# Optimization experiments

Hardware: AMD Instinct MI355X
Metric: run time of the kernel (lower is better)

Reference implementation:

```python
import jax, jax.numpy as jnp
import numpy as np

MAX_PER_CLASS = 100   # max_num_boxes_per_class
MAX_TOTAL = 300       # max_num_boxes (pad_per_class=False -> output size is MAX_TOTAL)
IOU_THR = 0.5
SCORE_THR = 0.001
NEG = jnp.float32(-1e30)
EPS = 1e-12


def _canon(b):
    # boxes given as any diagonal pair (y1,x1,y2,x2); canonicalize like TF NMS
    ymin = jnp.minimum(b[..., 0], b[..., 2])
    ymax = jnp.maximum(b[..., 0], b[..., 2])
    xmin = jnp.minimum(b[..., 1], b[..., 3])
    xmax = jnp.maximum(b[..., 1], b[..., 3])
    return ymin, xmin, ymax, xmax


def _iou_one_vs_all(box, boxes):
    # box [4], boxes [N,4] -> iou [N]
    y1a, x1a, y2a, x2a = _canon(box)
    y1b, x1b, y2b, x2b = _canon(boxes)
    ih = jnp.maximum(jnp.minimum(y2a, y2b) - jnp.maximum(y1a, y1b), 0.0)
    iw = jnp.maximum(jnp.minimum(x2a, x2b) - jnp.maximum(x1a, x1b), 0.0)
    inter = ih * iw
    area_a = (y2a - y1a) * (x2a - x1a)
    area_b = (y2b - y1b) * (x2b - x1b)
    union = jnp.maximum(area_a + area_b - inter, EPS)
    return inter / union


def _nms_single_class(boxes_c, scores_c):
    # boxes_c [N,4], scores_c [N] -> (scores [K], boxes [K,4], valid [K]) with K=MAX_PER_CLASS
    N = scores_c.shape[0]
    valid = scores_c > SCORE_THR
    s = jnp.where(valid, scores_c, NEG)
    order = jnp.argsort(-s)
    b_sorted = boxes_c[order]          # [N,4]
    s_sorted = s[order]                # [N]
    v_sorted = valid[order]            # [N]

    def step(keep, xs):
        i, box_i, valid_i = xs
        iou_row = _iou_one_vs_all(box_i, b_sorted)          # [N]
        suppressed = jnp.any(keep & (iou_row > IOU_THR))    # vs previously kept only
        keep = keep.at[i].set(valid_i & jnp.logical_not(suppressed))
        return keep, None

    keep0 = jnp.zeros((N,), dtype=bool)
    keep, _ = jax.lax.scan(step, keep0, (jnp.arange(N), b_sorted, v_sorted))

    # cap number of kept boxes at MAX_PER_CLASS (in descending score order)
    rank = jnp.cumsum(keep.astype(jnp.int32)) - 1
    keep = keep & (rank < MAX_PER_CLASS)

    key = jnp.where(keep, s_sorted, NEG)
    top_s, top_i = jax.lax.top_k(key, MAX_PER_CLASS)
    top_boxes = b_sorted[top_i]
    top_valid = top_s > (NEG / 2)
    return top_s, top_boxes, top_valid


def _combined_nms(scores, boxes):
    # scores [B,N,C], boxes [B,N,q,4] with q==1 (boxes shared across classes)
    B, N, C = scores.shape
    q = boxes.shape[2]

    def per_image(scores_i, boxes_i):
        # scores_i [N,C], boxes_i [N,q,4]
        if q == 1:
            cls_boxes = jnp.broadcast_to(boxes_i, (N, C, 4))
        else:
            cls_boxes = boxes_i
        # per-class NMS, vmapped over the class axis
        sc, bx, vd = jax.vmap(_nms_single_class, in_axes=(1, 1))(cls_boxes, scores_i)
        # sc [C,K], bx [C,K,4], vd [C,K]
        cls_ids = jnp.broadcast_to(
            jnp.arange(C, dtype=scores.dtype)[:, None], vd.shape)

        flat_s = jnp.where(vd, sc, NEG).reshape(-1)   # [C*K]
        flat_b = bx.reshape(-1, 4)
        flat_c = cls_ids.reshape(-1)
        flat_v = vd.reshape(-1)

        top_s, idx = jax.lax.top_k(flat_s, MAX_TOTAL)
        out_v = flat_v[idx]
        out_s = jnp.where(out_v, top_s, 0.0)
        out_b = jnp.where(out_v[:, None], flat_b[idx], 0.0)
        out_b = jnp.clip(out_b, 0.0, 1.0)             # clip_boxes=True
        out_c = jnp.where(out_v, flat_c[idx], 0.0)
        count = jnp.sum(out_v.astype(jnp.int32))
        return out_s, out_b, out_c, count

    return jax.vmap(per_image)(scores, boxes)


def setup_inputs() -> dict:
    key = jax.random.key(0)
    k1, k2 = jax.random.split(key)
    B, N, C, Q = 4, 1024, 80, 1
    scores = jax.random.uniform(k1, (B, N, C), dtype=jnp.float32)
    boxes = jax.random.uniform(k2, (B, N, Q, 4), dtype=jnp.float32)
    return {"scores": scores, "boxes": boxes}


def reference(scores, boxes):
    # returns (output_scores, output_boxes, output_classes, valid_counts)
    return _combined_nms(scores, boxes)
```

## Files before the change

### kernel.cpp

```cpp
#include <hip/hip_runtime.h>
#include <stdint.h>

#define N_BOX 1024
#define C_CLS 80
#define B_IMG 4
#define K_PER 100
#define K_TOT 300
#define NEGF  (-1e30f)
#define NCAND (C_CLS * K_PER)
#define M_SEL 8192
#define KPAD  1088

#define OFF_WSCORE  1835008
#define OFF_WSIDX   1963008

typedef unsigned long long u64;
typedef unsigned int u32;

__device__ __forceinline__ int swz(int i) { return i + (i >> 4); }

__device__ __forceinline__ u32 ford(float f) {
    u32 u = __float_as_uint(f);
    return (u & 0x80000000u) ? ~u : (u | 0x80000000u);
}
__device__ __forceinline__ float funord(u32 o) {
    u32 u = (o & 0x80000000u) ? (o ^ 0x80000000u) : ~o;
    return __uint_as_float(u);
}

__device__ __forceinline__ bool iou_gt(float4 a, float aa, float4 b, float ab) {
#pragma clang fp contract(off)
    float ih = fminf(a.z, b.z) - fmaxf(a.x, b.x); ih = fmaxf(ih, 0.0f);
    float iw = fminf(a.w, b.w) - fmaxf(a.y, b.y); iw = fmaxf(iw, 0.0f);
    float inter = ih * iw;
    float uni = fmaxf(aa + ab - inter, 1e-12f);
    return (inter / uni) > 0.5f;
}

__global__ __launch_bounds__(256, 2) void nms_classes(
        const float* __restrict__ scores,
        const float* __restrict__ boxes,
        float* __restrict__ ws_score,
        int*   __restrict__ ws_idx)
{
    __shared__ u64    key[KPAD];
    __shared__ float4 bx[N_BOX];
    __shared__ float  ar[N_BOX];
    __shared__ float4 kb[K_PER];
    __shared__ float  ka[K_PER];
    __shared__ int    kept_t[K_PER];
    __shared__ u32    colk32[64][2];
    __shared__ u32    suppw[2];
    __shared__ int    sh_nvalid, sh_kept;

    const int tid  = threadIdx.x;
    const int lane = tid & 63;
    const int b  = blockIdx.x / C_CLS;
    const int c  = blockIdx.x % C_CLS;

    if (tid == 0) { sh_nvalid = 0; sh_kept = 0; }

    for (int n = tid; n < N_BOX; n += 256) {
        float4 v = ((const float4*)boxes)[b * N_BOX + n];
        {
#pragma clang fp contract(off)
            float y1 = fminf(v.x, v.z), y2 = fmaxf(v.x, v.z);
            float x1 = fminf(v.y, v.w), x2 = fmaxf(v.y, v.w);
            bx[n] = make_float4(y1, x1, y2, x2);
            ar[n] = (y2 - y1) * (x2 - x1);
        }
    }
    __syncthreads();

    u64 r[4];
    {
        const float* sc = scores + (size_t)(b * N_BOX) * C_CLS + c;
        int lv = 0;
        #pragma unroll
        for (int q = 0; q < 4; ++q) {
            int v = tid * 4 + q;
            float s0 = sc[(size_t)v * C_CLS];
            bool valid = s0 > 0.001f;
            float s = valid ? s0 : NEGF;
            r[q] = ((u64)ford(s) << 32) | (u32)(N_BOX - 1 - v);
            lv += valid ? 1 : 0;
        }
        if (lv) atomicAdd(&sh_nvalid, lv);
    }

    #define CE(a, b, d) { u64 _mx = (a) > (b) ? (a) : (b); \
                          u64 _mn = (a) > (b) ? (b) : (a); \
                          (a) = (d) ? _mx : _mn; (b) = (d) ? _mn : _mx; }
    CE(r[0], r[1], true); CE(r[2], r[3], false);

    for (int k = 4; k <= N_BOX; k <<= 1) {
        const bool d = ((tid & (k >> 2)) == 0);
        for (int j = k >> 1; j > 0; j >>= 1) {
            if (j >= 256) {
                __syncthreads();
                #pragma unroll
                for (int q = 0; q < 4; ++q) key[swz(tid * 4 + q)] = r[q];
                __syncthreads();
                const bool upper = ((tid * 4) & j) != 0;
                #pragma unroll
                for (int q = 0; q < 4; ++q) {
                    u64 pv = key[swz((tid * 4 + q) ^ j)];
                    u64 mx = r[q] > pv ? r[q] : pv;
                    u64 mn = r[q] > pv ? pv : r[q];
                    r[q] = (d != upper) ? mx : mn;
                }
            } else if (j >= 4) {
                const int dl = j >> 2;
                const bool upper = (lane & dl) != 0;
                #pragma unroll
                for (int q = 0; q < 4; ++q) {
                    u64 pv = __shfl_xor(r[q], dl);
                    u64 mx = r[q] > pv ? r[q] : pv;
                    u64 mn = r[q] > pv ? pv : r[q];
                    r[q] = (d != upper) ? mx : mn;
                }
            } else if (j == 2) {
                CE(r[0], r[2], d); CE(r[1], r[3], d);
            } else {
                CE(r[0], r[1], d); CE(r[2], r[3], d);
            }
        }
    }
    #undef CE

    __syncthreads();
    #pragma unroll
    for (int q = 0; q < 4; ++q) key[swz(tid * 4 + q)] = r[q];
    __syncthreads();

    const int nvalid = sh_nvalid;
    const int nwin = (nvalid + 63) >> 6;
    const int me  = tid & 63;
    const int grp = tid >> 6;

    for (int w = 0; w < nwin; ++w) {
        __syncthreads();
        if (sh_kept >= K_PER) break;
        const int kept0 = sh_kept;
        const int bt = w * 64;

        u64 kvm = key[swz((bt + me) & (N_BOX - 1))];
        int idxm = (N_BOX - 1) - (int)(u32)(kvm & 0xFFFFFFFFu);
        const float4 qm = bx[idxm];
        const float  am = ar[idxm];

        if (grp == 0) { colk32[me][0] = 0; colk32[me][1] = 0; }
        if (tid < 2) suppw[tid] = 0;
        __syncthreads();

        bool supme = false;
        for (int k = grp; k < kept0; k += 4)
            if (iou_gt(kb[k], ka[k], qm, am)) supme = true;
        if (supme) atomicOr(&suppw[me >> 5], 1u << (me & 31));

        u32 bits = 0;
        #pragma unroll
        for (int rq = 0; rq < 16; ++rq) {
            int rr = grp * 16 + rq;
            u64 kvr = key[swz((bt + rr) & (N_BOX - 1))];
            int idxr = (N_BOX - 1) - (int)(u32)(kvr & 0xFFFFFFFFu);
            bool kill = (rr != me) && iou_gt(bx[idxr], ar[idxr], qm, am);
            bits |= ((u32)kill) << rq;
        }
        atomicOr(&colk32[me][grp >> 1], bits << ((grp & 1) * 16));
        __syncthreads();

        if (grp == 0) {
            const u64 colkill = ((u64)colk32[lane][1] << 32) | colk32[lane][0];
            const u64 supp    = ((u64)suppw[1] << 32) | suppw[0];
            bool in = ((bt + lane) < nvalid) && !((supp >> lane) & 1ull);
            u64 pending = __ballot(in);
            int kept = kept0;
            while (pending && kept < K_PER) {
                int t0 = __ffsll((long long)pending) - 1;
                if (lane == 0) kept_t[kept] = bt + t0;
                if (lane == t0) { kb[kept] = qm; ka[kept] = am; }
                kept++;
                bool kill = (colkill >> t0) & 1ull;
                pending &= ~(1ull << t0);
                pending &= ~__ballot(kill);
            }
            if (lane == 0) sh_kept = kept;
        }
    }
    __syncthreads();

    const int kept = sh_kept;
    if (tid < K_PER) {
        int ob = (b * C_CLS + c) * K_PER + tid;
        if (tid < kept) {
            u64 k = key[swz(kept_t[tid])];
            ws_score[ob] = funord((u32)(k >> 32));
            ws_idx[ob]   = (N_BOX - 1) - (int)(u32)(k & 0xFFFFFFFFu);
        } else {
            ws_score[ob] = NEGF;
            ws_idx[ob]   = 0;
        }
    }
}

__global__ __launch_bounds__(1024) void final_topk(
        const float* __restrict__ ws_score,
        const int*   __restrict__ ws_idx,
        const float* __restrict__ boxes,
        float* __restrict__ out)
{
    __shared__ u32 skey[NCAND];
    __shared__ u32 hist4[256 * 4];
    __shared__ u64 list[512];
    __shared__ int sh_sel;
    __shared__ u32 sh_need;
    __shared__ int sh_cnt, sh_valid;

    const int tid = threadIdx.x;
    const int b = blockIdx.x;
    const int base = b * NCAND;

    if (tid == 0) { sh_cnt = 0; sh_valid = 0; }
    for (int i = tid; i < NCAND; i += 1024)
        skey[i] = ford(ws_score[base + i]);
    if (tid < 512) list[tid] = 0;
    hist4[tid] = 0;
    __syncthreads();

    u64 prefix = 0;
    u32 need = K_TOT;
    const int rounds[6] = {7, 6, 5, 4, 1, 0};
    const int slot = tid & 3;

    for (int rd = 0; rd < 6; ++rd) {
        const int d = rounds[rd];
        for (int i = tid; i < NCAND; i += 1024) {
            u64 k = ((u64)skey[i] << 32) | (u32)(M_SEL - 1 - i);
            bool match = (d == 7) || (((k ^ prefix) >> (8 * (d + 1))) == 0);
            if (match)
                atomicAdd(&hist4[(((u32)(k >> (8 * d)) & 0xFFu) << 2) | slot], 1u);
        }
        __syncthreads();
        if (tid < 64) {
            const int l = tid;
            u32 h[4];
            #pragma unroll
            for (int q = 0; q < 4; ++q) {
                int bin = 4 * l + q;
                h[q] = hist4[bin * 4 + 0] + hist4[bin * 4 + 1]
                     + hist4[bin * 4 + 2] + hist4[bin * 4 + 3];
                hist4[bin * 4 + 0] = 0; hist4[bin * 4 + 1] = 0;
                hist4[bin * 4 + 2] = 0; hist4[bin * 4 + 3] = 0;
            }
            u32 s3 = h[3], s2 = h[2] + s3, s1 = h[1] + s2, s0 = h[0] + s1;
            u32 tot = s0, S = tot;
            #pragma unroll
            for (int off = 1; off < 64; off <<= 1) {
                u32 t = __shfl(S, (l + off) & 63);
                if (l + off < 64) S += t;
            }
            u32 T = S - tot;
            u32 sv0 = s0 + T, sv1 = s1 + T, sv2 = s2 + T, sv3 = s3 + T;
            if (sv0 >= need && sv1 < need) { sh_sel = 4*l;     sh_need = need - sv1; }
            if (sv1 >= need && sv2 < need) { sh_sel = 4*l + 1; sh_need = need - sv2; }
            if (sv2 >= need && sv3 < need) { sh_sel = 4*l + 2; sh_need = need - sv3; }
            if (sv3 >= need && T   < need) { sh_sel = 4*l + 3; sh_need = need - T;   }
        }
        __syncthreads();
        prefix |= ((u64)(u32)sh_sel) << (8 * d);
        need = sh_need;
        __syncthreads();
    }

    for (int i = tid; i < NCAND; i += 1024) {
        u64 k = ((u64)skey[i] << 32) | (u32)(M_SEL - 1 - i);
        if (k >= prefix) {
            int p = atomicAdd(&sh_cnt, 1);
            if (p < 512) list[p] = k;
        }
    }
    __syncthreads();

    if (tid < 64) {
        const int l = tid;
        u64 e[8];
        #pragma unroll
        for (int q = 0; q < 8; ++q) e[q] = list[l * 8 + q];
        #define CE2(a, b, dd) { u64 _mx = (a) > (b) ? (a) : (b); \
                                u64 _mn = (a) > (b) ? (b) : (a); \
                                (a) = (dd) ? _mx : _mn; (b) = (dd) ? _mn : _mx; }
        CE2(e[0], e[1], true);  CE2(e[2], e[3], false);
        CE2(e[4], e[5], true);  CE2(e[6], e[7], false);
        CE2(e[0], e[2], true);  CE2(e[1], e[3], true);
        CE2(e[4], e[6], false); CE2(e[5], e[7], false);
        CE2(e[0], e[1], true);  CE2(e[2], e[3], true);
        CE2(e[4], e[5], false); CE2(e[6], e[7], false);
        for (int k = 8; k <= 512; k <<= 1) {
            const bool d = ((l & (k >> 3)) == 0);
            for (int j = k >> 1; j >= 8; j >>= 1) {
                const int dl = j >> 3;
                const bool upper = (l & dl) != 0;
                #pragma unroll
                for (int q = 0; q < 8; ++q) {
                    u64 pv = __shfl_xor(e[q], dl);
                    u64 mx = e[q] > pv ? e[q] : pv;
                    u64 mn = e[q] > pv ? pv : e[q];
                    e[q] = (d != upper) ? mx : mn;
                }
            }
            CE2(e[0], e[4], d); CE2(e[1], e[5], d);
            CE2(e[2], e[6], d); CE2(e[3], e[7], d);
            CE2(e[0], e[2], d); CE2(e[1], e[3], d);
            CE2(e[4], e[6], d); CE2(e[5], e[7], d);
            CE2(e[0], e[1], d); CE2(e[2], e[3], d);
            CE2(e[4], e[5], d); CE2(e[6], e[7], d);
        }
        #undef CE2
        #pragma unroll
        for (int q = 0; q < 8; ++q) list[l * 8 + q] = e[q];
    }
    __syncthreads();

    float* out_s = out;
    float* out_b = out + B_IMG * K_TOT;
    float* out_c = out + B_IMG * K_TOT * 5;
    float* out_n = out + B_IMG * K_TOT * 6;

    for (int i = tid; i < K_TOT; i += 1024) {
        u64 k = list[i];
        float s = funord((u32)(k >> 32));
        int flat = (M_SEL - 1) - (int)(u32)(k & 0xFFFFFFFFu);
        bool valid = s > (-5e29f);
        float os = 0.0f, oc = 0.0f;
        float4 ob = make_float4(0.0f, 0.0f, 0.0f, 0.0f);
        if (valid && flat < NCAND) {
            int cc = flat / K_PER;
            int n  = ws_idx[base + flat];
            float4 bb = ((const float4*)boxes)[b * N_BOX + n];
            os = s;
            oc = (float)cc;
            ob.x = fminf(fmaxf(bb.x, 0.0f), 1.0f);
            ob.y = fminf(fmaxf(bb.y, 0.0f), 1.0f);
            ob.z = fminf(fmaxf(bb.z, 0.0f), 1.0f);
            ob.w = fminf(fmaxf(bb.w, 0.0f), 1.0f);
            atomicAdd(&sh_valid, 1);
        }
        out_s[b * K_TOT + i] = os;
        ((float4*)out_b)[b * K_TOT + i] = ob;
        out_c[b * K_TOT + i] = oc;
    }
    __syncthreads();
    if (tid == 0) out_n[b] = (float)sh_valid;
}

extern "C" void kernel_launch(void* const* d_in, const int* in_sizes, int n_in,
                              void* d_out, int out_size, void* d_ws, size_t ws_size,
                              hipStream_t stream) {
    const float* scores = (const float*)d_in[0];
    const float* boxes  = (const float*)d_in[1];

    char* ws = (char*)d_ws;
    float* ws_score = (float*)(ws + OFF_WSCORE);
    int*   ws_idx   = (int*)  (ws + OFF_WSIDX);

    nms_classes<<<dim3(B_IMG * C_CLS), dim3(256), 0, stream>>>(
        scores, boxes, ws_score, ws_idx);
    final_topk<<<dim3(B_IMG), dim3(1024), 0, stream>>>(
        ws_score, ws_idx, boxes, (float*)d_out);
}
```

Baseline: 121.0 us.

## Double-buffer window boxes and replace shared atomics with ballots

Gathers the next window's sorted boxes into a double-buffered shared array while the current window runs, so the indirect key-to-box lookups leave the critical loop. Shared-memory atomics and the zeroing pass for the kill and suppress masks are replaced by per-wave plain stores and wave ballots, which removes one barrier per window. The suppression check against kept boxes is batched into groups of eight loads. The goal is fewer barriers and less LDS latency per window, in exchange for more shared memory and more register pressure.

```diff
diff --git a/kernel.cpp b/kernel.cpp
--- a/kernel.cpp
+++ b/kernel.cpp
@@ -46,11 +46,13 @@
     __shared__ u64    key[KPAD];
     __shared__ float4 bx[N_BOX];
     __shared__ float  ar[N_BOX];
-    __shared__ float4 kb[K_PER];
-    __shared__ float  ka[K_PER];
+    __shared__ float4 wb[2][64];
+    __shared__ float  wa[2][64];
+    __shared__ float4 kb[128];
+    __shared__ float  ka[128];
     __shared__ int    kept_t[K_PER];
-    __shared__ u32    colk32[64][2];
-    __shared__ u32    suppw[2];
+    __shared__ u32    colk16[4][64];
+    __shared__ u64    sup64[4];
     __shared__ int    sh_nvalid, sh_kept;
 
     const int tid  = threadIdx.x;
@@ -133,46 +135,78 @@
     for (int q = 0; q < 4; ++q) key[swz(tid * 4 + q)] = r[q];
     __syncthreads();
 
+    if (tid < 64) {
+        u64 kv = key[swz(tid)];
+        int idx = (N_BOX - 1) - (int)(u32)(kv & 0xFFFFFFFFu);
+        wb[0][tid] = bx[idx];
+        wa[0][tid] = ar[idx];
+    }
+
     const int nvalid = sh_nvalid;
     const int nwin = (nvalid + 63) >> 6;
     const int me  = tid & 63;
     const int grp = tid >> 6;
 
     for (int w = 0; w < nwin; ++w) {
+        const int cur = w & 1;
         __syncthreads();
         if (sh_kept >= K_PER) break;
         const int kept0 = sh_kept;
         const int bt = w * 64;
 
-        u64 kvm = key[swz((bt + me) & (N_BOX - 1))];
-        int idxm = (N_BOX - 1) - (int)(u32)(kvm & 0xFFFFFFFFu);
-        const float4 qm = bx[idxm];
-        const float  am = ar[idxm];
-
-        if (grp == 0) { colk32[me][0] = 0; colk32[me][1] = 0; }
-        if (tid < 2) suppw[tid] = 0;
+        if (grp == 1 && (w + 1) < nwin) {
+            u64 kv = key[swz((bt + 64 + me) & (N_BOX - 1))];
+            int idx = (N_BOX - 1) - (int)(u32)(kv & 0xFFFFFFFFu);
+            wb[cur ^ 1][me] = bx[idx];
+            wa[cur ^ 1][me] = ar[idx];
+        }
+
+        const float4 qm = wb[cur][me];
+        const float  am = wa[cur][me];
+
+        {
+            float4 wrow[16]; float warow[16];
+            #pragma unroll
+            for (int rq = 0; rq < 16; ++rq) {
+                wrow[rq]  = wb[cur][grp * 16 + rq];
+                warow[rq] = wa[cur][grp * 16 + rq];
+            }
+            u32 bits = 0;
+            #pragma unroll
+            for (int rq = 0; rq < 16; ++rq) {
+                int rr = grp * 16 + rq;
+                bool kill = (rr != me) && iou_gt(wrow[rq], warow[rq], qm, am);
+                bits |= ((u32)kill) << rq;
+            }
+            colk16[grp][me] = bits;
+        }
+
+        {
+            bool supme = false;
+            for (int t0 = 0; grp + 4 * t0 < kept0; t0 += 8) {
+                float4 kbl[8]; float kal[8];
+                #pragma unroll
+                for (int i = 0; i < 8; ++i) {
+                    int k = grp + 4 * (t0 + i);
+                    kbl[i] = kb[k]; kal[i] = ka[k];
+                }
+                #pragma unroll
+                for (int i = 0; i < 8; ++i) {
+                    int k = grp + 4 * (t0 + i);
+                    if (k < kept0 && iou_gt(kbl[i], kal[i], qm, am)) supme = true;
+                }
+            }
+            u64 bal = __ballot(supme);
+            if (lane == 0) sup64[grp] = bal;
+        }
         __syncthreads();
 
-        bool supme = false;
-        for (int k = grp; k < kept0; k += 4)
-            if (iou_gt(kb[k], ka[k], qm, am)) supme = true;
-        if (supme) atomicOr(&suppw[me >> 5], 1u << (me & 31));
-
-        u32 bits = 0;
-        #pragma unroll
-        for (int rq = 0; rq < 16; ++rq) {
-            int rr = grp * 16 + rq;
-            u64 kvr = key[swz((bt + rr) & (N_BOX - 1))];
-            int idxr = (N_BOX - 1) - (int)(u32)(kvr & 0xFFFFFFFFu);
-            bool kill = (rr != me) && iou_gt(bx[idxr], ar[idxr], qm, am);
-            bits |= ((u32)kill) << rq;
-        }
-        atomicOr(&colk32[me][grp >> 1], bits << ((grp & 1) * 16));
-        __syncthreads();
-
         if (grp == 0) {
-            const u64 colkill = ((u64)colk32[lane][1] << 32) | colk32[lane][0];
-            const u64 supp    = ((u64)suppw[1] << 32) | suppw[0];
+            u32 c0 = colk16[0][lane], c1 = colk16[1][lane];
+            u32 c2 = colk16[2][lane], c3 = colk16[3][lane];
+            u64 colkill = (u64)c0 | ((u64)c1 << 16)
+                        | ((u64)c2 << 32) | ((u64)c3 << 48);
+            u64 supp = sup64[0] | sup64[1] | sup64[2] | sup64[3];
             bool in = ((bt + lane) < nvalid) && !((supp >> lane) & 1ull);
             u64 pending = __ballot(in);
             int kept = kept0;
```

After: 117.0 us. 1.03x faster.
